# Optimization experiments

Hardware: AMD Instinct MI355X
Metric: run time of the kernel (lower is better)

## Reference

```python
import jax, jax.numpy as jnp
import numpy as np
import math

B, C, H, W = 16, 128, 64, 64

def _conv3(x, w, b):
    # 3x3 conv, padding=1 (SAME), NCHW / OIHW
    y = jax.lax.conv_general_dilated(x, w, window_strides=(1, 1), padding='SAME',
                                     dimension_numbers=('NCHW', 'OIHW', 'NCHW'))
    return y + b[None, :, None, None]

def setup_inputs() -> dict:
    key = jax.random.key(0)
    ks = jax.random.split(key, 12)
    s = 0.02
    inp = {
        'F_in': jax.random.normal(ks[0], (B, C, H, W), dtype=jnp.float32),
        'Pspe': jax.random.normal(ks[1], (B, C, C), dtype=jnp.float32),
        'q_w': jax.random.normal(ks[2], (C, C, 3, 3), dtype=jnp.float32) * s,
        'q_b': jnp.zeros((C,), dtype=jnp.float32),
        'k_w': jax.random.normal(ks[3], (C, C, 3, 3), dtype=jnp.float32) * s,
        'k_b': jnp.zeros((C,), dtype=jnp.float32),
        'v_w': jax.random.normal(ks[4], (C, C, 3, 3), dtype=jnp.float32) * s,
        'v_b': jnp.zeros((C,), dtype=jnp.float32),
        'f1_w': jax.random.normal(ks[5], (C, C, 3, 3), dtype=jnp.float32) * s,
        'f1_b': jnp.zeros((C,), dtype=jnp.float32),
        'f2_w': jax.random.normal(ks[6], (C, C, 3, 3), dtype=jnp.float32) * s,
        'f2_b': jnp.zeros((C,), dtype=jnp.float32),
    }
    return inp

def reference(F_in, Pspe, q_w, q_b, k_w, k_b, v_w, v_b, f1_w, f1_b, f2_w, f2_b):
    b, c, h, w = F_in.shape
    hw = h * w
    Qm = _conv3(F_in, q_w, q_b)
    Km = _conv3(F_in, k_w, k_b)
    Vm = _conv3(F_in, v_w, v_b)
    # (B,C,H,W) -> (B,HW,C)
    Q = jnp.transpose(Qm, (0, 2, 3, 1)).reshape(b, hw, c)
    K = jnp.transpose(Km, (0, 2, 3, 1)).reshape(b, hw, c)
    V = jnp.transpose(Vm, (0, 2, 3, 1)).reshape(b, hw, c)
    # channel-wise attention: (B,C,C) = K^T Q, contracting over HW
    attn_logits = jnp.einsum('bnc,bnd->bcd', K, Q) / math.sqrt(hw)
    A = jax.nn.softmax(attn_logits, axis=-1)
    M = jnp.einsum('bce,bed->bcd', Pspe, A)         # prompt fusion
    F3 = jnp.einsum('bnc,bcd->bnd', V, M)           # (B,HW,C)
    F3_map = jnp.transpose(F3.reshape(b, h, w, c), (0, 3, 1, 2))
    # MScanBlock is not defined in the provided source -> identity
    F_ssm = F3_map
    ffn = _conv3(jax.nn.gelu(_conv3(F_ssm, f1_w, f1_b), approximate=False), f2_w, f2_b)
    return F_ssm + ffn
```

## Files before the change

### kernel.cpp

```cpp
#include <hip/hip_runtime.h>
#include <cmath>

typedef unsigned short u16;
typedef __bf16 bf16x8 __attribute__((ext_vector_type(8)));
typedef float f32x4 __attribute__((ext_vector_type(4)));

__device__ __forceinline__ u16 f2bf(float f) {
  unsigned u = __float_as_uint(f);
  u += 0x7fffu + ((u >> 16) & 1u);
  return (u16)(u >> 16);
}
__device__ __forceinline__ float bf2f(u16 h) {
  return __uint_as_float(((unsigned)h) << 16);
}
__device__ __forceinline__ f32x4 mfma_bf16(bf16x8 a, bf16x8 b, f32x4 c) {
  return __builtin_amdgcn_mfma_f32_16x16x32_bf16(a, b, c, 0, 0, 0);
}
__device__ __forceinline__ float gelu_exact(float x) {
  return 0.5f * x * (1.0f + erff(x * 0.70710678118654752440f));
}

__device__ __forceinline__ void gload16(const void* g, void* l) {
  __builtin_amdgcn_global_load_lds(
      (const __attribute__((address_space(1))) unsigned*)g,
      (__attribute__((address_space(3))) unsigned*)l, 16, 0, 0);
}

__device__ __forceinline__ size_t pidx(int b, int y, int x) {
  return ((size_t)(b * 66 + y) * 66 + x) * 128;
}

__device__ __forceinline__ void border_yx(int k, int& y, int& x) {
  if (k < 66) { y = 0; x = k; }
  else if (k < 132) { y = 65; x = k - 66; }
  else if (k < 196) { y = k - 131; x = 0; }
  else { y = k - 195; x = 65; }
}

__global__ __launch_bounds__(256) void pack_xw(
    const float* __restrict__ Fin, u16* __restrict__ Xp,
    const float* __restrict__ w0, const float* __restrict__ w1,
    const float* __restrict__ w2, const float* __restrict__ w3,
    const float* __restrict__ w4, u16* __restrict__ Wpk) {
  const int tid = threadIdx.x;
  const int bid = blockIdx.x;
  if (bid < 1024) {
    __shared__ float T[64 * 129];
    const int b = bid >> 6, y = bid & 63;
#pragma unroll
    for (int i = 0; i < 32; ++i) {
      int idx = tid + i * 256;
      int c = idx >> 6, x = idx & 63;
      T[x * 129 + c] = Fin[(size_t)(b * 128 + c) * 4096 + y * 64 + x];
    }
    __syncthreads();
#pragma unroll
    for (int i = 0; i < 4; ++i) {
      int chunk = tid + i * 256;
      int x = chunk >> 4;
      int c0 = (chunk & 15) * 8;
      u16 tmp[8];
#pragma unroll
      for (int e = 0; e < 8; ++e) tmp[e] = f2bf(T[x * 129 + c0 + e]);
      *reinterpret_cast<uint4*>(Xp + pidx(b, y + 1, x + 1) + c0) =
          *reinterpret_cast<const uint4*>(tmp);
    }
  } else if (bid < 1384) {
    int gid = (bid - 1024) * 256 + tid;
    int lane = gid & 63;
    int nblk = (gid >> 6) & 7;
    int step = (gid >> 9) % 36;
    int conv = gid / (512 * 36);
    if (conv >= 5) return;
    const float* w = conv == 0 ? w0 : conv == 1 ? w1 : conv == 2 ? w2 : conv == 3 ? w3 : w4;
    int tap = step >> 2, cc = step & 3;
    int dy = tap / 3, dx = tap % 3;
    int co = nblk * 16 + (lane & 15);
    int ci0 = cc * 32 + (lane >> 4) * 8;
    u16 tmp[8];
#pragma unroll
    for (int e = 0; e < 8; ++e)
      tmp[e] = f2bf(w[((size_t)(co * 128 + ci0 + e) * 3 + dy) * 3 + dx]);
    size_t off = ((size_t)conv * 36 * 8 * 64 + (size_t)((step * 8 + nblk) * 64 + lane)) * 8;
    *reinterpret_cast<uint4*>(Wpk + off) = *reinterpret_cast<const uint4*>(tmp);
  } else {
    int p = (bid - 1384) * 16 + (tid >> 4);
    int b = p / 260, k = p % 260;
    int y, x;
    border_yx(k, y, x);
    *reinterpret_cast<uint4*>(Xp + pidx(b, y, x) + (tid & 15) * 8) =
        make_uint4(0u, 0u, 0u, 0u);
  }
}

template <int MODE, int NS>
__global__ __launch_bounds__(256, 4) void conv5(
    const u16* __restrict__ Xin, const u16* __restrict__ Wp0,
    const float* __restrict__ bq, const float* __restrict__ bk,
    const float* __restrict__ bv,
    u16* __restrict__ O0, u16* __restrict__ O1, u16* __restrict__ O2,
    float* __restrict__ OutF, const u16* __restrict__ Resid) {
  constexpr int NBJ = 4 / NS;
  __shared__ alignas(16) char smem[MODE == 0 ? 34816 : 33792];
  char* Abuf = smem;
  const int tid = threadIdx.x;
  const int lane = tid & 63, wv = tid >> 6;
  const int wm = wv >> 1, wn = wv & 1;
  const int lm = lane & 15, lq = lane >> 4;
  const int bid = blockIdx.x;
  const int cv = (MODE == 0) ? (bid >> 9) : 0;
  const int nh = (NS == 2) ? (bid & 1) : 0;
  const int mtr = (MODE == 0) ? (bid & 511) : (bid >> 1);
  const int mt = (mtr & 7) * 64 + (mtr >> 3);
  const int b = mt >> 5, yp = mt & 31;
  const u16* WpC = Wp0 + (size_t)cv * 147456;
  const int cb0 = nh * 4 + wn * NBJ;
  const u16* wlane = WpC + (size_t)cb0 * 512 + (size_t)lane * 8;

  f32x4 acc[4][NBJ];
#pragma unroll
  for (int i = 0; i < 4; ++i)
#pragma unroll
    for (int j = 0; j < NBJ; ++j) acc[i][j] = f32x4{0.f, 0.f, 0.f, 0.f};

  auto stageA = [&](int h) {
#pragma unroll
    for (int r = 0; r < 9; ++r) {
      int c = wv * 528 + r * 64 + lane;
      int row = c >> 3, c16 = c & 7;
      int ys = row / 66, xs = row - ys * 66;
      const u16* src =
          Xin + pidx(b, yp * 2 + ys, xs) + h * 64 + ((c16 ^ (xs & 7)) << 3);
      char* dst = Abuf + (wv * 528 + r * 64) * 16;
      if (r < 8)
        gload16(src, dst);
      else if (lane < 16)
        gload16(src, dst);
    }
  };

#pragma unroll 1
  for (int h = 0; h < 2; ++h) {
    __syncthreads();
    stageA(h);
    __syncthreads();
#pragma unroll
    for (int t = 0; t < 18; ++t) {
      const int tap = t >> 1, ccL = t & 1;
      const int dy = tap / 3, dx = tap - dy * 3;
      const int ws = tap * 4 + h * 2 + ccL;
      const int ysrow = (wm + dy) * 8448;
      const int q0 = ccL * 4 + lq;
      bf16x8 af[4], bfr[NBJ];
#pragma unroll
      for (int i = 0; i < 4; ++i) {
        int xs = i * 16 + lm + dx;
        int off = ysrow + xs * 128 + ((q0 ^ (xs & 7)) << 4);
        af[i] = *reinterpret_cast<const bf16x8*>(Abuf + off);
      }
#pragma unroll
      for (int j = 0; j < NBJ; ++j)
        bfr[j] = *reinterpret_cast<const bf16x8*>(wlane + ws * 4096 + j * 512);
#pragma unroll
      for (int i = 0; i < 4; ++i)
#pragma unroll
        for (int j = 0; j < NBJ; ++j)
          acc[i][j] = mfma_bf16(af[i], bfr[j], acc[i][j]);
    }
  }

  __syncthreads();

  if (MODE == 0 && cv < 2) {
    const float* bias = cv == 0 ? bq : bk;
    u16* OutB = cv == 0 ? O0 : O1;
    u16* T = (u16*)smem;
#pragma unroll
    for (int i = 0; i < 4; ++i)
#pragma unroll
      for (int j = 0; j < NBJ; ++j) {
        int n = wn * 64 + j * 16 + lm;
        float bs = bias[n];
#pragma unroll
        for (int r = 0; r < 4; ++r) {
          int m = wm * 64 + i * 16 + lq * 4 + r;
          T[n * 136 + m] = f2bf(acc[i][j][r] + bs);
        }
      }
    __syncthreads();
#pragma unroll
    for (int it = 0; it < 8; ++it) {
      int item = tid + it * 256;
      int l = item & 63, cb = (item >> 6) & 7, ksl = item >> 9;
      int c = cb * 16 + (l & 15);
      int mloc = ksl * 32 + (l >> 4) * 8;
      int ks = yp * 4 + ksl;
      *reinterpret_cast<uint4*>(
          OutB + (size_t)(((b * 128 + ks) * 8 + cb) * 64 + l) * 8) =
          *reinterpret_cast<const uint4*>(T + c * 136 + mloc);
    }
  } else if (MODE == 0) {
    u16* T = (u16*)smem;
#pragma unroll
    for (int i = 0; i < 4; ++i)
#pragma unroll
      for (int j = 0; j < NBJ; ++j) {
        int n = wn * 64 + j * 16 + lm;
        float bs = bv[n];
#pragma unroll
        for (int r = 0; r < 4; ++r) {
          int m = wm * 64 + i * 16 + lq * 4 + r;
          T[m * 136 + n] = f2bf(acc[i][j][r] + bs);
        }
      }
    __syncthreads();
    int rr = tid >> 1, hf = tid & 1;
    const uint4* src = reinterpret_cast<const uint4*>(T + rr * 136 + hf * 64);
    uint4* dst = reinterpret_cast<uint4*>(O2 + ((size_t)(mt * 128 + rr) * 128 + hf * 64));
#pragma unroll
    for (int k = 0; k < 8; ++k) dst[k] = src[k];
  } else if (MODE == 1) {
    u16* T = (u16*)smem;
#pragma unroll
    for (int i = 0; i < 4; ++i)
#pragma unroll
      for (int j = 0; j < NBJ; ++j) {
        int nloc = wn * 32 + j * 16 + lm;
        float bs = bq[nh * 64 + nloc];
#pragma unroll
        for (int r = 0; r < 4; ++r) {
          int m = wm * 64 + i * 16 + lq * 4 + r;
          T[m * 72 + nloc] = f2bf(gelu_exact(acc[i][j][r] + bs));
        }
      }
    __syncthreads();
    int rr = tid >> 1, q = tid & 1;
    int y = yp * 2 + (rr >> 6), x = rr & 63;
    const uint4* src = reinterpret_cast<const uint4*>(T + rr * 72 + q * 32);
    uint4* dst =
        reinterpret_cast<uint4*>(O0 + pidx(b, y + 1, x + 1) + nh * 64 + q * 32);
#pragma unroll
    for (int k = 0; k < 4; ++k) dst[k] = src[k];
  } else {
    float* Tf = (float*)smem;
#pragma unroll
    for (int i = 0; i < 4; ++i)
#pragma unroll
      for (int j = 0; j < NBJ; ++j) {
        int nl = wn * 32 + j * 16 + lm;
        int n = nh * 64 + nl;
        float bs = bq[n];
        int m0 = wm * 64 + i * 16 + lq * 4;
        int y = yp * 2 + (m0 >> 6), x = m0 & 63;
        const u16* rp = Resid + pidx(b, y + 1, x + 1) + n;
#pragma unroll
        for (int r = 0; r < 4; ++r)
          Tf[nl * 132 + m0 + r] = acc[i][j][r] + bs + bf2f(rp[r * 128]);
      }
    __syncthreads();
    int nl = tid >> 2, seg = tid & 3;
    float* dst = OutF + ((size_t)(b * 128 + nh * 64 + nl) * 4096 + yp * 128 + seg * 32);
    const float* src = Tf + nl * 132 + seg * 32;
#pragma unroll
    for (int k = 0; k < 8; ++k)
      reinterpret_cast<float4*>(dst)[k] = reinterpret_cast<const float4*>(src)[k];
  }
}

__global__ __launch_bounds__(256, 2) void attn_s(const u16* __restrict__ QP,
                                                 const u16* __restrict__ KP,
                                                 float* __restrict__ SP) {
  const int tid = threadIdx.x;
  const int lane = tid & 63;
  const int wv = tid >> 6, wm = wv >> 1, wn = wv & 1;
  const int lm = lane & 15, lq = lane >> 4;
  int mt = blockIdx.x;
  mt = (mt & 7) * 16 + (mt >> 3);
  const int b = mt >> 3, sp = mt & 7;

  f32x4 acc[4][4];
#pragma unroll
  for (int i = 0; i < 4; ++i)
#pragma unroll
    for (int j = 0; j < 4; ++j) acc[i][j] = f32x4{0.f, 0.f, 0.f, 0.f};

#pragma unroll
  for (int ksl = 0; ksl < 16; ++ksl) {
    const int ks = sp * 16 + ksl;
    bf16x8 af[4], bfr[4];
#pragma unroll
    for (int i = 0; i < 4; ++i)
      af[i] = *reinterpret_cast<const bf16x8*>(
          KP + (size_t)(((b * 128 + ks) * 8 + wm * 4 + i) * 64 + lane) * 8);
#pragma unroll
    for (int j = 0; j < 4; ++j)
      bfr[j] = *reinterpret_cast<const bf16x8*>(
          QP + (size_t)(((b * 128 + ks) * 8 + wn * 4 + j) * 64 + lane) * 8);
#pragma unroll
    for (int i = 0; i < 4; ++i)
#pragma unroll
      for (int j = 0; j < 4; ++j) acc[i][j] = mfma_bf16(af[i], bfr[j], acc[i][j]);
  }

  float* out = SP + (size_t)(b * 8 + sp) * 16384;
#pragma unroll
  for (int i = 0; i < 4; ++i)
#pragma unroll
    for (int j = 0; j < 4; ++j)
#pragma unroll
      for (int r = 0; r < 4; ++r)
        out[(wm * 64 + i * 16 + lq * 4 + r) * 128 + wn * 64 + j * 16 + lm] =
            acc[i][j][r];
}

__global__ __launch_bounds__(256) void attn_r(const float* __restrict__ SP,
                                              u16* __restrict__ ABP) {
  __shared__ float Sf[32][129];
  __shared__ float Inv[32];
  const int tid = threadIdx.x;
  const int b = blockIdx.x >> 2, eb = blockIdx.x & 3;

#pragma unroll
  for (int it = 0; it < 16; ++it) {
    int id = it * 256 + tid;
    int rl = id >> 7, d = id & 127;
    const float* p = SP + (size_t)b * 8 * 16384 + (size_t)(eb * 32 + rl) * 128 + d;
    float s = 0.f;
#pragma unroll
    for (int sp = 0; sp < 8; ++sp) s += p[(size_t)sp * 16384];
    Sf[rl][d] = s * 0.015625f;
  }
  __syncthreads();

  {
    int rl = tid >> 3, sub = tid & 7;
    float mx = -3.4e38f;
#pragma unroll
    for (int k = 0; k < 16; ++k) mx = fmaxf(mx, Sf[rl][sub + 8 * k]);
    mx = fmaxf(mx, __shfl_xor(mx, 1));
    mx = fmaxf(mx, __shfl_xor(mx, 2));
    mx = fmaxf(mx, __shfl_xor(mx, 4));
    float s = 0.f;
#pragma unroll
    for (int k = 0; k < 16; ++k) {
      float e = __expf(Sf[rl][sub + 8 * k] - mx);
      Sf[rl][sub + 8 * k] = e;
      s += e;
    }
    s += __shfl_xor(s, 1);
    s += __shfl_xor(s, 2);
    s += __shfl_xor(s, 4);
    if (sub == 0) Inv[rl] = 1.0f / s;
  }
  __syncthreads();

#pragma unroll
  for (int it = 0; it < 2; ++it) {
    int item = tid + it * 256;
    int l = item & 63, nb = item >> 6;
    int d = nb * 16 + (l & 15);
    u16 tmp[8];
#pragma unroll
    for (int e = 0; e < 8; ++e) {
      int rloc = (l >> 4) * 8 + e;
      tmp[e] = f2bf(Sf[rloc][d] * Inv[rloc]);
    }
    *reinterpret_cast<uint4*>(ABP + (size_t)(((b * 4 + eb) * 8 + nb) * 64 + l) * 8) =
        *reinterpret_cast<const uint4*>(tmp);
  }
}

__global__ __launch_bounds__(256, 1) void attn_m(const float* __restrict__ Pspe,
                                                 const u16* __restrict__ ABP,
                                                 u16* __restrict__ Mpack) {
  __shared__ u16 Ml[128 * 136];
  const int b = blockIdx.x;
  const int tid = threadIdx.x;
  const int lane = tid & 63;
  const int wv = tid >> 6, wm = wv >> 1, wn = wv & 1;
  const int lm = lane & 15, lq = lane >> 4;

  f32x4 acc[4][4];
#pragma unroll
  for (int i = 0; i < 4; ++i)
#pragma unroll
    for (int j = 0; j < 4; ++j) acc[i][j] = f32x4{0.f, 0.f, 0.f, 0.f};

  const float* P = Pspe + (size_t)b * 128 * 128;
#pragma unroll
  for (int cc = 0; cc < 4; ++cc) {
    int e0 = cc * 32 + lq * 8;
    bf16x8 af[4], bfr[4];
#pragma unroll
    for (int i = 0; i < 4; ++i) {
      const float* p = P + (size_t)(wm * 64 + i * 16 + lm) * 128 + e0;
      union { u16 u[8]; bf16x8 v; } cvu;
#pragma unroll
      for (int e = 0; e < 8; ++e) cvu.u[e] = f2bf(p[e]);
      af[i] = cvu.v;
    }
#pragma unroll
    for (int j = 0; j < 4; ++j)
      bfr[j] = *reinterpret_cast<const bf16x8*>(
          ABP + (size_t)(((b * 4 + cc) * 8 + wn * 4 + j) * 64 + lane) * 8);
#pragma unroll
    for (int i = 0; i < 4; ++i)
#pragma unroll
      for (int j = 0; j < 4; ++j) acc[i][j] = mfma_bf16(af[i], bfr[j], acc[i][j]);
  }

#pragma unroll
  for (int i = 0; i < 4; ++i)
#pragma unroll
    for (int j = 0; j < 4; ++j)
#pragma unroll
      for (int r = 0; r < 4; ++r)
        Ml[(wn * 64 + j * 16 + lm) * 136 + (wm * 64 + i * 16 + lq * 4 + r)] =
            f2bf(acc[i][j][r]);
  __syncthreads();

#pragma unroll
  for (int it = 0; it < 8; ++it) {
    int item = tid + it * 256;
    int l2 = item & 63, nb = (item >> 6) & 7, cc2 = item >> 9;
    int d = nb * 16 + (l2 & 15), c0 = cc2 * 32 + (l2 >> 4) * 8;
    *reinterpret_cast<uint4*>(Mpack + (size_t)b * 16384 + (size_t)item * 8) =
        *reinterpret_cast<const uint4*>(Ml + d * 136 + c0);
  }
}

__global__ __launch_bounds__(256) void f3_gemm(const u16* __restrict__ V,
                                               const u16* __restrict__ Mpack,
                                               u16* __restrict__ Fp,
                                               u16* __restrict__ Hp) {
  const int tid = threadIdx.x;
  const int lane = tid & 63;
  const int wv = tid >> 6, wm = wv >> 1, wn = wv & 1;
  const int lm = lane & 15, lq = lane >> 4;
  const int bid = blockIdx.x;
  int mt = bid;
  mt = (mt & 7) * 64 + (mt >> 3);
  const int b = mt >> 5;
  const int yp = mt & 31;

  f32x4 acc[4][4];
#pragma unroll
  for (int i = 0; i < 4; ++i)
#pragma unroll
    for (int j = 0; j < 4; ++j) acc[i][j] = f32x4{0.f, 0.f, 0.f, 0.f};

#pragma unroll
  for (int cc = 0; cc < 4; ++cc) {
    int k0 = cc * 32 + lq * 8;
    bf16x8 af[4], bfr[4];
#pragma unroll
    for (int i = 0; i < 4; ++i)
      af[i] = *reinterpret_cast<const bf16x8*>(
          V + (size_t)(mt * 128 + wm * 64 + i * 16 + lm) * 128 + k0);
#pragma unroll
    for (int j = 0; j < 4; ++j)
      bfr[j] = *reinterpret_cast<const bf16x8*>(
          Mpack + (size_t)b * 16384 + (size_t)((cc * 8 + wn * 4 + j) * 64 + lane) * 8);
#pragma unroll
    for (int i = 0; i < 4; ++i)
#pragma unroll
      for (int j = 0; j < 4; ++j) acc[i][j] = mfma_bf16(af[i], bfr[j], acc[i][j]);
  }

#pragma unroll
  for (int rep = 0; rep < 2; ++rep) {
    int p = bid * 32 + rep * 16 + (tid >> 4);
    if (p < 8320) {
      u16* buf = p < 4160 ? Fp : Hp;
      int q = p < 4160 ? p : p - 4160;
      int bb = q / 260, k = q % 260;
      int y, x;
      border_yx(k, y, x);
      *reinterpret_cast<uint4*>(buf + pidx(bb, y, x) + (tid & 15) * 8) =
          make_uint4(0u, 0u, 0u, 0u);
    }
  }

  __shared__ u16 T[128 * 136];
#pragma unroll
  for (int i = 0; i < 4; ++i)
#pragma unroll
    for (int j = 0; j < 4; ++j)
#pragma unroll
      for (int r = 0; r < 4; ++r)
        T[(wm * 64 + i * 16 + lq * 4 + r) * 136 + wn * 64 + j * 16 + lm] =
            f2bf(acc[i][j][r]);
  __syncthreads();
  int rr = tid >> 1, hf = tid & 1;
  int y = yp * 2 + (rr >> 6), x = rr & 63;
  const uint4* src = reinterpret_cast<const uint4*>(T + rr * 136 + hf * 64);
  uint4* dst = reinterpret_cast<uint4*>(Fp + pidx(b, y + 1, x + 1) + hf * 64);
#pragma unroll
  for (int k = 0; k < 8; ++k) dst[k] = src[k];
}

extern "C" void kernel_launch(void* const* d_in, const int* in_sizes, int n_in,
                              void* d_out, int out_size, void* d_ws, size_t ws_size,
                              hipStream_t stream) {
  const float* F_in = (const float*)d_in[0];
  const float* Pspe = (const float*)d_in[1];
  const float* q_w = (const float*)d_in[2];
  const float* q_b = (const float*)d_in[3];
  const float* k_w = (const float*)d_in[4];
  const float* k_b = (const float*)d_in[5];
  const float* v_w = (const float*)d_in[6];
  const float* v_b = (const float*)d_in[7];
  const float* f1_w = (const float*)d_in[8];
  const float* f1_b = (const float*)d_in[9];
  const float* f2_w = (const float*)d_in[10];
  const float* f2_b = (const float*)d_in[11];
  float* out = (float*)d_out;

  char* ws = (char*)d_ws;
  const size_t XPO = 0;
  const size_t QPO = 17842176;
  const size_t KPO = QPO + 16777216;
  const size_t VO  = KPO + 16777216;
  const size_t WPO = VO + 16777216;

  u16* Xp = (u16*)(ws + XPO);
  u16* QP = (u16*)(ws + QPO);
  u16* KP = (u16*)(ws + KPO);
  u16* V = (u16*)(ws + VO);
  u16* Wpk = (u16*)(ws + WPO);
  float* SP = (float*)(ws + XPO);
  u16* ABP = KP;
  u16* Mpk = (u16*)(ws + KPO + 1179648);
  u16* Fp = Xp;
  u16* Hp = QP;

  pack_xw<<<1644, 256, 0, stream>>>(F_in, Xp, q_w, k_w, v_w, f1_w, f2_w, Wpk);
  conv5<0, 1><<<1536, 256, 0, stream>>>(Xp, Wpk, q_b, k_b, v_b, QP, KP, V,
                                        nullptr, nullptr);
  attn_s<<<128, 256, 0, stream>>>(QP, KP, SP);
  attn_r<<<64, 256, 0, stream>>>(SP, ABP);
  attn_m<<<16, 256, 0, stream>>>(Pspe, ABP, Mpk);
  f3_gemm<<<512, 256, 0, stream>>>(V, Mpk, Fp, Hp);
  conv5<1, 2><<<1024, 256, 0, stream>>>(Fp, Wpk + 3 * 147456, f1_b, nullptr,
                                        nullptr, Hp, nullptr, nullptr, nullptr,
                                        nullptr);
  conv5<2, 2><<<1024, 256, 0, stream>>>(Hp, Wpk + 4 * 147456, f2_b, nullptr,
                                        nullptr, nullptr, nullptr, nullptr, out,
                                        Fp);
}
```

Measured before the change: 196.6 us.

## Share staged input tile across QKV convs and fuse softmax with prompt GEMM

The conv kernel now stages the full 128-channel input halo tile once into 66KB of shared memory. In the QKV mode one block computes all three convolutions from that tile, and each block covers all 128 output channels instead of splitting them across blocks, so the input is loaded once rather than three or six times. Separately, the softmax kernel and the Pspe×A kernel are merged into one 16-block kernel that keeps A transposed in shared memory, removing one launch and a global round trip. MFMA issue gets setprio hints. In exchange occupancy drops to 2 blocks per CU, the QKV grid shrinks to 512 blocks, and each thread holds 48 accumulators.

```diff
diff --git a/kernel.cpp b/kernel.cpp
--- a/kernel.cpp
+++ b/kernel.cpp
@@ -93,124 +93,126 @@
   }
 }
 
-template <int MODE, int NS>
-__global__ __launch_bounds__(256, 4) void conv5(
-    const u16* __restrict__ Xin, const u16* __restrict__ Wp0,
-    const float* __restrict__ bq, const float* __restrict__ bk,
-    const float* __restrict__ bv,
-    u16* __restrict__ O0, u16* __restrict__ O1, u16* __restrict__ O2,
-    float* __restrict__ OutF, const u16* __restrict__ Resid) {
-  constexpr int NBJ = 4 / NS;
-  __shared__ alignas(16) char smem[MODE == 0 ? 34816 : 33792];
-  char* Abuf = smem;
+__device__ __forceinline__ void stageA_full(const u16* __restrict__ Xp, char* Xs,
+                                            int tid, int b, int y0p) {
+#pragma unroll
+  for (int i = 0; i < 17; ++i) {
+    if (i == 16 && tid >= 128) break;
+    int j = i * 256 + tid;
+    int row = j >> 4, c16 = j & 15;
+    int ys = row / 66, xs = row - ys * 66;
+    const u16* src = Xp + pidx(b, y0p + ys, xs) + ((c16 ^ (xs & 7)) << 3);
+    gload16(src, Xs + j * 16);
+  }
+}
+
+template <int MODE>
+__global__ __launch_bounds__(256, 2) void convX(
+    const u16* __restrict__ Xin, const u16* __restrict__ Wp,
+    const float* __restrict__ b0, const float* __restrict__ b1,
+    const float* __restrict__ b2, u16* __restrict__ O0, u16* __restrict__ O1,
+    u16* __restrict__ O2, float* __restrict__ OutF,
+    const u16* __restrict__ Resid) {
+  constexpr int NCV = (MODE == 0) ? 3 : 1;
+  __shared__ alignas(16) char smem[67584];
   const int tid = threadIdx.x;
   const int lane = tid & 63, wv = tid >> 6;
   const int wm = wv >> 1, wn = wv & 1;
+  int mt = blockIdx.x;
+  mt = (mt & 7) * 64 + (mt >> 3);
+  const int b = mt >> 5, yp = mt & 31;
   const int lm = lane & 15, lq = lane >> 4;
-  const int bid = blockIdx.x;
-  const int cv = (MODE == 0) ? (bid >> 9) : 0;
-  const int nh = (NS == 2) ? (bid & 1) : 0;
-  const int mtr = (MODE == 0) ? (bid & 511) : (bid >> 1);
-  const int mt = (mtr & 7) * 64 + (mtr >> 3);
-  const int b = mt >> 5, yp = mt & 31;
-  const u16* WpC = Wp0 + (size_t)cv * 147456;
-  const int cb0 = nh * 4 + wn * NBJ;
-  const u16* wlane = WpC + (size_t)cb0 * 512 + (size_t)lane * 8;
-
-  f32x4 acc[4][NBJ];
-#pragma unroll
-  for (int i = 0; i < 4; ++i)
-#pragma unroll
-    for (int j = 0; j < NBJ; ++j) acc[i][j] = f32x4{0.f, 0.f, 0.f, 0.f};
-
-  auto stageA = [&](int h) {
-#pragma unroll
-    for (int r = 0; r < 9; ++r) {
-      int c = wv * 528 + r * 64 + lane;
-      int row = c >> 3, c16 = c & 7;
-      int ys = row / 66, xs = row - ys * 66;
-      const u16* src =
-          Xin + pidx(b, yp * 2 + ys, xs) + h * 64 + ((c16 ^ (xs & 7)) << 3);
-      char* dst = Abuf + (wv * 528 + r * 64) * 16;
-      if (r < 8)
-        gload16(src, dst);
-      else if (lane < 16)
-        gload16(src, dst);
-    }
-  };
+
+  stageA_full(Xin, smem, tid, b, yp * 2);
+  __syncthreads();
+
+  f32x4 acc[NCV][4][4];
+#pragma unroll
+  for (int c = 0; c < NCV; ++c)
+#pragma unroll
+    for (int i = 0; i < 4; ++i)
+#pragma unroll
+      for (int j = 0; j < 4; ++j) acc[c][i][j] = f32x4{0.f, 0.f, 0.f, 0.f};
+
+  const u16* wlane = Wp + (size_t)lane * 8;
 
 #pragma unroll 1
-  for (int h = 0; h < 2; ++h) {
-    __syncthreads();
-    stageA(h);
-    __syncthreads();
-#pragma unroll
-    for (int t = 0; t < 18; ++t) {
-      const int tap = t >> 1, ccL = t & 1;
-      const int dy = tap / 3, dx = tap - dy * 3;
-      const int ws = tap * 4 + h * 2 + ccL;
-      const int ysrow = (wm + dy) * 8448;
-      const int q0 = ccL * 4 + lq;
-      bf16x8 af[4], bfr[NBJ];
+  for (int tap = 0; tap < 9; ++tap) {
+    const int dy = (tap * 11) >> 5;
+    const int dx = tap - dy * 3;
+#pragma unroll
+    for (int cc = 0; cc < 4; ++cc) {
+      const int step = tap * 4 + cc;
+      bf16x8 af[4];
 #pragma unroll
       for (int i = 0; i < 4; ++i) {
         int xs = i * 16 + lm + dx;
-        int off = ysrow + xs * 128 + ((q0 ^ (xs & 7)) << 4);
-        af[i] = *reinterpret_cast<const bf16x8*>(Abuf + off);
+        unsigned off = (unsigned)((((wm + dy) * 66 + xs) * 128 + cc * 32 + lq * 8) * 2) ^
+                       (unsigned)((xs & 7) << 4);
+        af[i] = *reinterpret_cast<const bf16x8*>(smem + off);
       }
 #pragma unroll
-      for (int j = 0; j < NBJ; ++j)
-        bfr[j] = *reinterpret_cast<const bf16x8*>(wlane + ws * 4096 + j * 512);
+      for (int cv = 0; cv < NCV; ++cv) {
+        bf16x8 bfr[4];
+#pragma unroll
+        for (int j = 0; j < 4; ++j)
+          bfr[j] = *reinterpret_cast<const bf16x8*>(
+              wlane + (size_t)cv * 147456 + (size_t)((step * 8 + wn * 4 + j) * 64) * 8);
+        __builtin_amdgcn_s_setprio(1);
+#pragma unroll
+        for (int i = 0; i < 4; ++i)
+#pragma unroll
+          for (int j = 0; j < 4; ++j)
+            acc[cv][i][j] = mfma_bf16(af[i], bfr[j], acc[cv][i][j]);
+        __builtin_amdgcn_s_setprio(0);
+      }
+    }
+  }
+
+  __syncthreads();
+
+  if (MODE == 0) {
+    u16* T = (u16*)smem;
+#pragma unroll 1
+    for (int cv = 0; cv < 2; ++cv) {
+      const float* bias = cv == 0 ? b0 : b1;
+      u16* OutB = cv == 0 ? O0 : O1;
 #pragma unroll
       for (int i = 0; i < 4; ++i)
 #pragma unroll
-        for (int j = 0; j < NBJ; ++j)
-          acc[i][j] = mfma_bf16(af[i], bfr[j], acc[i][j]);
-    }
-  }
-
-  __syncthreads();
-
-  if (MODE == 0 && cv < 2) {
-    const float* bias = cv == 0 ? bq : bk;
-    u16* OutB = cv == 0 ? O0 : O1;
-    u16* T = (u16*)smem;
-#pragma unroll
-    for (int i = 0; i < 4; ++i)
-#pragma unroll
-      for (int j = 0; j < NBJ; ++j) {
+        for (int j = 0; j < 4; ++j) {
+          int n = wn * 64 + j * 16 + lm;
+          float bs = bias[n];
+#pragma unroll
+          for (int r = 0; r < 4; ++r) {
+            int m = wm * 64 + i * 16 + lq * 4 + r;
+            T[n * 136 + m] = f2bf(acc[cv][i][j][r] + bs);
+          }
+        }
+      __syncthreads();
+#pragma unroll
+      for (int it = 0; it < 8; ++it) {
+        int item = tid + it * 256;
+        int l = item & 63, cb = (item >> 6) & 7, ksl = item >> 9;
+        int c = cb * 16 + (l & 15);
+        int mloc = ksl * 32 + (l >> 4) * 8;
+        int ks = yp * 4 + ksl;
+        *reinterpret_cast<uint4*>(
+            OutB + (size_t)(((b * 128 + ks) * 8 + cb) * 64 + l) * 8) =
+            *reinterpret_cast<const uint4*>(T + c * 136 + mloc);
+      }
+      __syncthreads();
+    }
+#pragma unroll
+    for (int i = 0; i < 4; ++i)
+#pragma unroll
+      for (int j = 0; j < 4; ++j) {
         int n = wn * 64 + j * 16 + lm;
-        float bs = bias[n];
+        float bs = b2[n];
 #pragma unroll
         for (int r = 0; r < 4; ++r) {
           int m = wm * 64 + i * 16 + lq * 4 + r;
-          T[n * 136 + m] = f2bf(acc[i][j][r] + bs);
-        }
-      }
-    __syncthreads();
-#pragma unroll
-    for (int it = 0; it < 8; ++it) {
-      int item = tid + it * 256;
-      int l = item & 63, cb = (item >> 6) & 7, ksl = item >> 9;
-      int c = cb * 16 + (l & 15);
-      int mloc = ksl * 32 + (l >> 4) * 8;
-      int ks = yp * 4 + ksl;
-      *reinterpret_cast<uint4*>(
-          OutB + (size_t)(((b * 128 + ks) * 8 + cb) * 64 + l) * 8) =
-          *reinterpret_cast<const uint4*>(T + c * 136 + mloc);
-    }
-  } else if (MODE == 0) {
-    u16* T = (u16*)smem;
-#pragma unroll
-    for (int i = 0; i < 4; ++i)
-#pragma unroll
-      for (int j = 0; j < NBJ; ++j) {
-        int n = wn * 64 + j * 16 + lm;
-        float bs = bv[n];
-#pragma unroll
-        for (int r = 0; r < 4; ++r) {
-          int m = wm * 64 + i * 16 + lq * 4 + r;
-          T[m * 136 + n] = f2bf(acc[i][j][r] + bs);
+          T[m * 136 + n] = f2bf(acc[2][i][j][r] + bs);
         }
       }
     __syncthreads();
@@ -224,45 +226,43 @@
 #pragma unroll
     for (int i = 0; i < 4; ++i)
 #pragma unroll
-      for (int j = 0; j < NBJ; ++j) {
-        int nloc = wn * 32 + j * 16 + lm;
-        float bs = bq[nh * 64 + nloc];
+      for (int j = 0; j < 4; ++j) {
+        int n = wn * 64 + j * 16 + lm;
+        float bs = b0[n];
 #pragma unroll
         for (int r = 0; r < 4; ++r) {
           int m = wm * 64 + i * 16 + lq * 4 + r;
-          T[m * 72 + nloc] = f2bf(gelu_exact(acc[i][j][r] + bs));
+          T[m * 136 + n] = f2bf(gelu_exact(acc[0][i][j][r] + bs));
         }
       }
     __syncthreads();
-    int rr = tid >> 1, q = tid & 1;
+    int rr = tid >> 1, hf = tid & 1;
     int y = yp * 2 + (rr >> 6), x = rr & 63;
-    const uint4* src = reinterpret_cast<const uint4*>(T + rr * 72 + q * 32);
-    uint4* dst =
-        reinterpret_cast<uint4*>(O0 + pidx(b, y + 1, x + 1) + nh * 64 + q * 32);
-#pragma unroll
-    for (int k = 0; k < 4; ++k) dst[k] = src[k];
+    const uint4* src = reinterpret_cast<const uint4*>(T + rr * 136 + hf * 64);
+    uint4* dst = reinterpret_cast<uint4*>(O0 + pidx(b, y + 1, x + 1) + hf * 64);
+#pragma unroll
+    for (int k = 0; k < 8; ++k) dst[k] = src[k];
   } else {
     float* Tf = (float*)smem;
 #pragma unroll
     for (int i = 0; i < 4; ++i)
 #pragma unroll
-      for (int j = 0; j < NBJ; ++j) {
-        int nl = wn * 32 + j * 16 + lm;
-        int n = nh * 64 + nl;
-        float bs = bq[n];
+      for (int j = 0; j < 4; ++j) {
+        int n = wn * 64 + j * 16 + lm;
+        float bs = b0[n];
         int m0 = wm * 64 + i * 16 + lq * 4;
         int y = yp * 2 + (m0 >> 6), x = m0 & 63;
         const u16* rp = Resid + pidx(b, y + 1, x + 1) + n;
 #pragma unroll
         for (int r = 0; r < 4; ++r)
-          Tf[nl * 132 + m0 + r] = acc[i][j][r] + bs + bf2f(rp[r * 128]);
+          Tf[n * 132 + m0 + r] = acc[0][i][j][r] + bs + bf2f(rp[r * 128]);
       }
     __syncthreads();
-    int nl = tid >> 2, seg = tid & 3;
-    float* dst = OutF + ((size_t)(b * 128 + nh * 64 + nl) * 4096 + yp * 128 + seg * 32);
-    const float* src = Tf + nl * 132 + seg * 32;
-#pragma unroll
-    for (int k = 0; k < 8; ++k)
+    int n2 = tid >> 1, seg = tid & 1;
+    float* dst = OutF + ((size_t)(b * 128 + n2) * 4096 + yp * 128 + seg * 64);
+    const float* src = Tf + n2 * 132 + seg * 64;
+#pragma unroll
+    for (int k = 0; k < 16; ++k)
       reinterpret_cast<float4*>(dst)[k] = reinterpret_cast<const float4*>(src)[k];
   }
 }
@@ -313,79 +313,55 @@
             acc[i][j][r];
 }
 
-__global__ __launch_bounds__(256) void attn_r(const float* __restrict__ SP,
-                                              u16* __restrict__ ABP) {
-  __shared__ float Sf[32][129];
-  __shared__ float Inv[32];
-  const int tid = threadIdx.x;
-  const int b = blockIdx.x >> 2, eb = blockIdx.x & 3;
-
-#pragma unroll
-  for (int it = 0; it < 16; ++it) {
-    int id = it * 256 + tid;
-    int rl = id >> 7, d = id & 127;
-    const float* p = SP + (size_t)b * 8 * 16384 + (size_t)(eb * 32 + rl) * 128 + d;
-    float s = 0.f;
-#pragma unroll
-    for (int sp = 0; sp < 8; ++sp) s += p[(size_t)sp * 16384];
-    Sf[rl][d] = s * 0.015625f;
-  }
-  __syncthreads();
-
-  {
-    int rl = tid >> 3, sub = tid & 7;
-    float mx = -3.4e38f;
-#pragma unroll
-    for (int k = 0; k < 16; ++k) mx = fmaxf(mx, Sf[rl][sub + 8 * k]);
-    mx = fmaxf(mx, __shfl_xor(mx, 1));
-    mx = fmaxf(mx, __shfl_xor(mx, 2));
-    mx = fmaxf(mx, __shfl_xor(mx, 4));
-    float s = 0.f;
-#pragma unroll
-    for (int k = 0; k < 16; ++k) {
-      float e = __expf(Sf[rl][sub + 8 * k] - mx);
-      Sf[rl][sub + 8 * k] = e;
-      s += e;
-    }
-    s += __shfl_xor(s, 1);
-    s += __shfl_xor(s, 2);
-    s += __shfl_xor(s, 4);
-    if (sub == 0) Inv[rl] = 1.0f / s;
-  }
-  __syncthreads();
-
-#pragma unroll
-  for (int it = 0; it < 2; ++it) {
-    int item = tid + it * 256;
-    int l = item & 63, nb = item >> 6;
-    int d = nb * 16 + (l & 15);
-    u16 tmp[8];
-#pragma unroll
-    for (int e = 0; e < 8; ++e) {
-      int rloc = (l >> 4) * 8 + e;
-      tmp[e] = f2bf(Sf[rloc][d] * Inv[rloc]);
-    }
-    *reinterpret_cast<uint4*>(ABP + (size_t)(((b * 4 + eb) * 8 + nb) * 64 + l) * 8) =
-        *reinterpret_cast<const uint4*>(tmp);
-  }
-}
-
-__global__ __launch_bounds__(256, 1) void attn_m(const float* __restrict__ Pspe,
-                                                 const u16* __restrict__ ABP,
-                                                 u16* __restrict__ Mpack) {
-  __shared__ u16 Ml[128 * 136];
+__global__ __launch_bounds__(256, 1) void attn_rm(const float* __restrict__ SP,
+                                                  const float* __restrict__ Pspe,
+                                                  u16* __restrict__ Mpack) {
+  __shared__ float Sf[128 * 129];
+  __shared__ u16 AT[128 * 136];
   const int b = blockIdx.x;
   const int tid = threadIdx.x;
   const int lane = tid & 63;
   const int wv = tid >> 6, wm = wv >> 1, wn = wv & 1;
   const int lm = lane & 15, lq = lane >> 4;
 
-  f32x4 acc[4][4];
+#pragma unroll
+  for (int it = 0; it < 64; ++it) {
+    int id = it * 256 + tid;
+    int rl = id >> 7, d = id & 127;
+    const float* p = SP + (size_t)b * 8 * 16384 + (size_t)rl * 128 + d;
+    float s = 0.f;
+#pragma unroll
+    for (int sp = 0; sp < 8; ++sp) s += p[(size_t)sp * 16384];
+    Sf[rl * 129 + d] = s * 0.015625f;
+  }
+  __syncthreads();
+
+  {
+    int c = tid >> 1, hf = tid & 1;
+    float* row = Sf + c * 129 + hf * 64;
+    float mx = -3.4e38f;
+#pragma unroll
+    for (int k = 0; k < 64; ++k) mx = fmaxf(mx, row[k]);
+    mx = fmaxf(mx, __shfl_xor(mx, 1));
+    float s = 0.f;
+#pragma unroll
+    for (int k = 0; k < 64; ++k) {
+      float e = __expf(row[k] - mx);
+      row[k] = e;
+      s += e;
+    }
+    s += __shfl_xor(s, 1);
+    float inv = 1.0f / s;
+#pragma unroll
+    for (int k = 0; k < 64; ++k) AT[(hf * 64 + k) * 136 + c] = f2bf(row[k] * inv);
+  }
+  __syncthreads();
+
+  f32x4 acc2[4][4];
 #pragma unroll
   for (int i = 0; i < 4; ++i)
 #pragma unroll
-    for (int j = 0; j < 4; ++j) acc[i][j] = f32x4{0.f, 0.f, 0.f, 0.f};
-
+    for (int j = 0; j < 4; ++j) acc2[i][j] = f32x4{0.f, 0.f, 0.f, 0.f};
   const float* P = Pspe + (size_t)b * 128 * 128;
 #pragma unroll
   for (int cc = 0; cc < 4; ++cc) {
@@ -394,21 +370,21 @@
 #pragma unroll
     for (int i = 0; i < 4; ++i) {
       const float* p = P + (size_t)(wm * 64 + i * 16 + lm) * 128 + e0;
-      union { u16 u[8]; bf16x8 v; } cvu;
-#pragma unroll
-      for (int e = 0; e < 8; ++e) cvu.u[e] = f2bf(p[e]);
-      af[i] = cvu.v;
+      union { u16 u[8]; bf16x8 v; } cvt;
+#pragma unroll
+      for (int e = 0; e < 8; ++e) cvt.u[e] = f2bf(p[e]);
+      af[i] = cvt.v;
     }
 #pragma unroll
     for (int j = 0; j < 4; ++j)
-      bfr[j] = *reinterpret_cast<const bf16x8*>(
-          ABP + (size_t)(((b * 4 + cc) * 8 + wn * 4 + j) * 64 + lane) * 8);
-#pragma unroll
-    for (int i = 0; i < 4; ++i)
-#pragma unroll
-      for (int j = 0; j < 4; ++j) acc[i][j] = mfma_bf16(af[i], bfr[j], acc[i][j]);
-  }
-
+      bfr[j] = *reinterpret_cast<const bf16x8*>(AT + (wn * 64 + j * 16 + lm) * 136 + e0);
+#pragma unroll
+    for (int i = 0; i < 4; ++i)
+#pragma unroll
+      for (int j = 0; j < 4; ++j) acc2[i][j] = mfma_bf16(af[i], bfr[j], acc2[i][j]);
+  }
+
+  u16* Ml = reinterpret_cast<u16*>(Sf);
 #pragma unroll
   for (int i = 0; i < 4; ++i)
 #pragma unroll
@@ -416,7 +392,7 @@
 #pragma unroll
       for (int r = 0; r < 4; ++r)
         Ml[(wn * 64 + j * 16 + lm) * 136 + (wm * 64 + i * 16 + lq * 4 + r)] =
-            f2bf(acc[i][j][r]);
+            f2bf(acc2[i][j][r]);
   __syncthreads();
 
 #pragma unroll
@@ -429,10 +405,10 @@
   }
 }
 
-__global__ __launch_bounds__(256) void f3_gemm(const u16* __restrict__ V,
-                                               const u16* __restrict__ Mpack,
-                                               u16* __restrict__ Fp,
-                                               u16* __restrict__ Hp) {
+__global__ __launch_bounds__(256, 4) void f3_gemm(const u16* __restrict__ V,
+                                                  const u16* __restrict__ Mpack,
+                                                  u16* __restrict__ Fp,
+                                                  u16* __restrict__ Hp) {
   const int tid = threadIdx.x;
   const int lane = tid & 63;
   const int wv = tid >> 6, wm = wv >> 1, wn = wv & 1;
@@ -529,22 +505,18 @@
   u16* V = (u16*)(ws + VO);
   u16* Wpk = (u16*)(ws + WPO);
   float* SP = (float*)(ws + XPO);
-  u16* ABP = KP;
   u16* Mpk = (u16*)(ws + KPO + 1179648);
   u16* Fp = Xp;
   u16* Hp = QP;
 
   pack_xw<<<1644, 256, 0, stream>>>(F_in, Xp, q_w, k_w, v_w, f1_w, f2_w, Wpk);
-  conv5<0, 1><<<1536, 256, 0, stream>>>(Xp, Wpk, q_b, k_b, v_b, QP, KP, V,
-                                        nullptr, nullptr);
+  convX<0><<<512, 256, 0, stream>>>(Xp, Wpk, q_b, k_b, v_b, QP, KP, V, nullptr,
+                                    nullptr);
   attn_s<<<128, 256, 0, stream>>>(QP, KP, SP);
-  attn_r<<<64, 256, 0, stream>>>(SP, ABP);
-  attn_m<<<16, 256, 0, stream>>>(Pspe, ABP, Mpk);
+  attn_rm<<<16, 256, 0, stream>>>(SP, Pspe, Mpk);
   f3_gemm<<<512, 256, 0, stream>>>(V, Mpk, Fp, Hp);
-  conv5<1, 2><<<1024, 256, 0, stream>>>(Fp, Wpk + 3 * 147456, f1_b, nullptr,
-                                        nullptr, Hp, nullptr, nullptr, nullptr,
-                                        nullptr);
-  conv5<2, 2><<<1024, 256, 0, stream>>>(Hp, Wpk + 4 * 147456, f2_b, nullptr,
-                                        nullptr, nullptr, nullptr, nullptr, out,
-                                        Fp);
-}
+  convX<1><<<512, 256, 0, stream>>>(Fp, Wpk + 3 * 147456, f1_b, nullptr, nullptr,
+                                    Hp, nullptr, nullptr, nullptr, nullptr);
+  convX<2><<<512, 256, 0, stream>>>(Hp, Wpk + 4 * 147456, f2_b, nullptr, nullptr,
+                                    nullptr, nullptr, nullptr, out, Fp);
+}
```

New measurement: 217.1 us. +10.5%, slower.
